# Optimization experiments

Hardware: AMD Instinct MI355X
Metric: run time of the kernel (lower is better)

## Reference

```python
import jax, jax.numpy as jnp
import numpy as np

VTH = 1.0          # firing threshold
SG_ALPHA = 4.0     # surrogate-gradient sharpness
TAU_MEM = 20.0

@jax.custom_vjp
def spike_fn(v):
    # Heaviside spike: 1 where membrane exceeds 0 (v is already v_mem - VTH)
    return (v > 0.0).astype(v.dtype)

def _spike_fwd(v):
    return spike_fn(v), v

def _spike_bwd(v, g):
    # sigmoid surrogate derivative: alpha * s * (1 - s)
    s = jax.nn.sigmoid(SG_ALPHA * v)
    return (g * SG_ALPHA * s * (1.0 - s),)

spike_fn.defvjp(_spike_fwd, _spike_bwd)

def lif_scan(h):
    # h: (batch, time, seq, hidden) -> spikes same shape, rate scalar
    beta = 1.0 - 1.0 / TAU_MEM  # membrane decay
    b, t, s, d = h.shape
    h_t = jnp.moveaxis(h, 1, 0)  # (time, batch, seq, hidden)

    def step(v, inp):
        v = beta * v + inp
        spk = spike_fn(v - VTH)
        v = v * (1.0 - spk)  # hard reset
        return v, spk

    v0 = jnp.zeros((b, s, d), dtype=h.dtype)
    _, spikes = jax.lax.scan(step, v0, h_t)
    spikes = jnp.moveaxis(spikes, 0, 1)  # (batch, time, seq, hidden)
    rate = spikes.mean()
    return spikes, rate

def setup_inputs() -> dict:
    key = jax.random.key(0)
    k1, k2, k3 = jax.random.split(key, 3)
    b, t, s, d = 16, 4, 256, 512
    hidden = 2048
    x = jax.random.normal(k1, (b, t, s, d), dtype=jnp.float32)
    # Kaiming-ish init so membrane inputs are O(1)
    w1 = jax.random.normal(k2, (hidden, d), dtype=jnp.float32) * (1.0 / np.sqrt(d))
    w2 = jax.random.normal(k3, (d, hidden), dtype=jnp.float32) * (1.0 / np.sqrt(hidden))
    return {"x": x, "w1": w1, "w2": w2}

def reference(x, w1, w2):
    # fc1: (b,t,s,d) @ (hidden,d)^T -> (b,t,s,hidden)
    h = jnp.einsum('btsd,hd->btsh', x, w1)
    spikes, rate = lif_scan(h)
    # fc2: (b,t,s,hidden) @ (d,hidden)^T -> (b,t,s,d)
    out = jnp.einsum('btsh,dh->btsd', spikes, w2)
    return out, rate
```

## Files before the change

kernel.cpp:

```cpp
#include <hip/hip_runtime.h>
#include <stdint.h>


typedef __attribute__((ext_vector_type(8))) short short8;
typedef __attribute__((ext_vector_type(4))) float f32x4;

#define AS1 __attribute__((address_space(1)))
#define AS3 __attribute__((address_space(3)))

__device__ __forceinline__ void load_lds16(const void* g, void* l) {
  __builtin_amdgcn_global_load_lds((const AS1 void*)g, (AS3 void*)l, 16, 0, 0);
}

__device__ __forceinline__ unsigned short f2bf(float f) {
  union { float f; unsigned u; } un; un.f = f;
  unsigned r = un.u + 0x7FFF + ((un.u >> 16) & 1);
  return (unsigned short)(r >> 16);
}
__device__ __forceinline__ float bf2f(unsigned short u) {
  union { unsigned u; float f; } un; un.u = ((unsigned)u) << 16; return un.f;
}

__global__ __launch_bounds__(256) void k0_split(
    const float* __restrict__ w2, unsigned short* __restrict__ hi,
    unsigned short* __restrict__ lo)
{
  int i = (blockIdx.x * 256 + threadIdx.x) * 4;
  float4 w = *(const float4*)&w2[i];
  unsigned short h4[4], l4[4];
  float ws[4] = {w.x, w.y, w.z, w.w};
#pragma unroll
  for (int c = 0; c < 4; ++c) {
    unsigned short h = f2bf(ws[c]);
    h4[c] = h;
    l4[c] = f2bf(ws[c] - bf2f(h));
  }
  *(ushort4*)&hi[i] = *(const ushort4*)h4;
  *(ushort4*)&lo[i] = *(const ushort4*)l4;
}

#define K1KT 32
#define SA_STR 256
#define SB_STR 128

__global__ __launch_bounds__(256, 2) void k1_gemm_lif(
    const float* __restrict__ x,
    const float* __restrict__ w1,
    unsigned short* __restrict__ spikes,
    unsigned* __restrict__ cnt_out)
{
  __shared__ float sA[K1KT * SA_STR];
  __shared__ float sB[K1KT * SB_STR];

  const int tid = threadIdx.x;
  const int tx  = tid & 15;
  const int ty  = tid >> 4;
  const int t   = ty & 3;
  const int ssg = ty >> 2;

  const int bx = blockIdx.x;
  const int b  = bx >> 2;
  const int s0 = (bx & 3) * 64;
  const int h0 = blockIdx.y * 128;

  const int u  = tid >> 3;
  const int kg = tid & 7;

  float acc[16][8];
#pragma unroll
  for (int i = 0; i < 16; ++i)
#pragma unroll
    for (int j = 0; j < 8; ++j) acc[i][j] = 0.0f;

  const int aBase  = t * 64 + ssg * 16;
  const int tXor   = 4 * t;
  const int bBase0 = tx * 4;
  const int bBase1 = 64 + tx * 4;

  for (int k0 = 0; k0 < 512; k0 += K1KT) {
    __syncthreads();

#pragma unroll
    for (int j = 0; j < 8; ++j) {
      int r  = u + 32 * j;
      int tr = r >> 6, ss = r & 63;
      size_t grow = ((size_t)(b * 4 + tr) << 8) + s0 + ss;
      float4 a = *(const float4*)&x[grow * 512 + k0 + kg * 4];
      int sl = r ^ (4 * (kg ^ tr));
      sA[(4 * kg + 0) * SA_STR + sl] = a.x;
      sA[(4 * kg + 1) * SA_STR + sl] = a.y;
      sA[(4 * kg + 2) * SA_STR + sl] = a.z;
      sA[(4 * kg + 3) * SA_STR + sl] = a.w;
    }
#pragma unroll
    for (int j = 0; j < 4; ++j) {
      int c = u + 32 * j;
      float4 wv = *(const float4*)&w1[(size_t)(h0 + c) * 512 + k0 + kg * 4];
      int sl = c ^ (4 * kg);
      sB[(4 * kg + 0) * SB_STR + sl] = wv.x;
      sB[(4 * kg + 1) * SB_STR + sl] = wv.y;
      sB[(4 * kg + 2) * SB_STR + sl] = wv.z;
      sB[(4 * kg + 3) * SB_STR + sl] = wv.w;
    }
    __syncthreads();

    for (int kk = 0; kk < K1KT; kk += 4) {
      const int aXor = kk ^ tXor;
      const int bXor = kk;
#pragma unroll
      for (int k2i = 0; k2i < 4; ++k2i) {
        const int k = kk + k2i;
        const float* aRow = &sA[k * SA_STR];
        const float* bRow = &sB[k * SB_STR];
        float4 a0 = *(const float4*)&aRow[(aBase + 0)  ^ aXor];
        float4 a1 = *(const float4*)&aRow[(aBase + 4)  ^ aXor];
        float4 a2 = *(const float4*)&aRow[(aBase + 8)  ^ aXor];
        float4 a3 = *(const float4*)&aRow[(aBase + 12) ^ aXor];
        float4 b0 = *(const float4*)&bRow[bBase0 ^ bXor];
        float4 b1 = *(const float4*)&bRow[bBase1 ^ bXor];
        float av[16] = {a0.x, a0.y, a0.z, a0.w, a1.x, a1.y, a1.z, a1.w,
                        a2.x, a2.y, a2.z, a2.w, a3.x, a3.y, a3.z, a3.w};
        float bv[8]  = {b0.x, b0.y, b0.z, b0.w, b1.x, b1.y, b1.z, b1.w};
#pragma unroll
        for (int i = 0; i < 16; ++i)
#pragma unroll
          for (int j = 0; j < 8; ++j)
            acc[i][j] = __builtin_fmaf(av[i], bv[j], acc[i][j]);
      }
    }
  }

  unsigned cnt = 0;
#pragma unroll
  for (int i = 0; i < 16; ++i) {
    unsigned short sp[8];
#pragma unroll
    for (int j = 0; j < 8; ++j) {
      float a = acc[i][j];
      float h[4];
#pragma unroll
      for (int tt = 0; tt < 4; ++tt)
        h[tt] = __shfl(a, tt * 16 + tx, 64);
      float vv = 0.0f;
      bool smine = false;
#pragma unroll
      for (int tt = 0; tt < 4; ++tt) {
        vv = __fadd_rn(__fmul_rn(0.95f, vv), h[tt]);
        bool s = vv > 1.0f;
        smine = (tt == t) ? s : smine;
        vv = s ? 0.0f : vv;
      }
      cnt += smine ? 1u : 0u;
      sp[j] = smine ? (unsigned short)0x3F80 : (unsigned short)0;
    }
    size_t grow = ((size_t)(b * 4 + t) << 8) + s0 + ssg * 16 + i;
    unsigned short* rowp = spikes + grow * 2048 + h0;
    *(ushort4*)&rowp[tx * 4]      = *(const ushort4*)&sp[0];
    *(ushort4*)&rowp[64 + tx * 4] = *(const ushort4*)&sp[4];
  }

#pragma unroll
  for (int off = 32; off; off >>= 1) cnt += __shfl_down(cnt, off);
  if ((tid & 63) == 0) atomicAdd(cnt_out, cnt);
}

__global__ __launch_bounds__(256, 2) void k2_gemm_mfma(
    const unsigned short* __restrict__ spikes,
    const unsigned short* __restrict__ w2h,
    const unsigned short* __restrict__ w2l,
    float* __restrict__ out)
{
  __shared__ alignas(16) short smA [128 * 64];
  __shared__ alignas(16) short smBh[128 * 64];
  __shared__ alignas(16) short smBl[128 * 64];

  const int tid  = threadIdx.x;
  const int lane = tid & 63;
  const int quad = lane >> 4;
  const int l15  = lane & 15;
  const int wv   = tid >> 6;
  const int wm   = wv & 1;
  const int wn   = wv >> 1;

  const size_t r0 = (size_t)blockIdx.x * 128;
  const int    d0 = blockIdx.y * 128;

  int srow[4], sg8[4];
#pragma unroll
  for (int j = 0; j < 4; ++j) {
    int gi  = j * 256 + tid;
    srow[j] = gi >> 3;
    sg8[j]  = ((gi & 7) ^ (srow[j] & 7)) * 8;
  }

  const unsigned short* ab  = spikes + r0 * 2048;
  const unsigned short* bhb = w2h + (size_t)d0 * 2048;
  const unsigned short* blb = w2l + (size_t)d0 * 2048;

  f32x4 acc[4][4] = {};

  for (int k0 = 0; k0 < 2048; k0 += 64) {
    __syncthreads();
#pragma unroll
    for (int j = 0; j < 4; ++j) {
      load_lds16(ab  + (size_t)srow[j] * 2048 + k0 + sg8[j],
                 &smA [(j * 256 + tid) * 8]);
      load_lds16(bhb + (size_t)srow[j] * 2048 + k0 + sg8[j],
                 &smBh[(j * 256 + tid) * 8]);
      load_lds16(blb + (size_t)srow[j] * 2048 + k0 + sg8[j],
                 &smBl[(j * 256 + tid) * 8]);
    }
    __syncthreads();

#pragma unroll
    for (int ks = 0; ks < 2; ++ks) {
      short8 af[4], bh[4], bl[4];
#pragma unroll
      for (int mi = 0; mi < 4; ++mi) {
        int m = wm * 64 + mi * 16 + l15;
        af[mi] = ((const short8*)smA)[m * 8 + ((ks * 4 + quad) ^ (m & 7))];
      }
#pragma unroll
      for (int ni = 0; ni < 4; ++ni) {
        int n = wn * 64 + ni * 16 + l15;
        int sl = n * 8 + ((ks * 4 + quad) ^ (n & 7));
        bh[ni] = ((const short8*)smBh)[sl];
        bl[ni] = ((const short8*)smBl)[sl];
      }
#pragma unroll
      for (int mi = 0; mi < 4; ++mi)
#pragma unroll
        for (int ni = 0; ni < 4; ++ni) {
          acc[mi][ni] = __builtin_amdgcn_mfma_f32_16x16x32_bf16(
              af[mi], bh[ni], acc[mi][ni], 0, 0, 0);
          acc[mi][ni] = __builtin_amdgcn_mfma_f32_16x16x32_bf16(
              af[mi], bl[ni], acc[mi][ni], 0, 0, 0);
        }
    }
  }

  float* ob = out + r0 * 512 + d0;
#pragma unroll
  for (int mi = 0; mi < 4; ++mi)
#pragma unroll
    for (int ni = 0; ni < 4; ++ni)
#pragma unroll
      for (int r = 0; r < 4; ++r) {
        int rr = wm * 64 + mi * 16 + quad * 4 + r;
        int cc = wn * 64 + ni * 16 + l15;
        ob[(size_t)rr * 512 + cc] = acc[mi][ni][r];
      }
}

#define KT 16
#define PADF 68

__global__ __launch_bounds__(256) void k2_gemm_valu(
    const unsigned short* __restrict__ spikes,
    const float* __restrict__ w2,
    float* __restrict__ out)
{
  __shared__ float sA[KT][PADF];
  __shared__ float sB[KT][PADF];

  const int tid = threadIdx.x;
  const int tx  = tid & 15;
  const int ty  = tid >> 4;
  const int lr  = tid >> 2;
  const int lg  = tid & 3;

  const size_t r0 = (size_t)blockIdx.x * 64;
  const int    d0 = blockIdx.y * 64;

  float acc[4][4];
#pragma unroll
  for (int i = 0; i < 4; ++i)
#pragma unroll
    for (int j = 0; j < 4; ++j) acc[i][j] = 0.0f;

  for (int k0 = 0; k0 < 2048; k0 += KT) {
    __syncthreads();
    ushort4 av = *(const ushort4*)&spikes[(r0 + lr) * 2048 + k0 + lg * 4];
    float4  bv = *(const float4*)&w2[(size_t)(d0 + lr) * 2048 + k0 + lg * 4];
    sA[lg * 4 + 0][lr] = bf2f(av.x); sA[lg * 4 + 1][lr] = bf2f(av.y);
    sA[lg * 4 + 2][lr] = bf2f(av.z); sA[lg * 4 + 3][lr] = bf2f(av.w);
    sB[lg * 4 + 0][lr] = bv.x; sB[lg * 4 + 1][lr] = bv.y;
    sB[lg * 4 + 2][lr] = bv.z; sB[lg * 4 + 3][lr] = bv.w;
    __syncthreads();

#pragma unroll
    for (int k = 0; k < KT; ++k) {
      float4 a4 = *(const float4*)&sA[k][ty * 4];
      float4 b4 = *(const float4*)&sB[k][tx * 4];
      float aa[4] = {a4.x, a4.y, a4.z, a4.w};
      float bb[4] = {b4.x, b4.y, b4.z, b4.w};
#pragma unroll
      for (int i = 0; i < 4; ++i)
#pragma unroll
        for (int j = 0; j < 4; ++j)
          acc[i][j] = __builtin_fmaf(aa[i], bb[j], acc[i][j]);
    }
  }

#pragma unroll
  for (int i = 0; i < 4; ++i) {
    float4 o = make_float4(acc[i][0], acc[i][1], acc[i][2], acc[i][3]);
    *(float4*)&out[(r0 + ty * 4 + i) * 512 + d0 + tx * 4] = o;
  }
}

__global__ void k3_rate(const unsigned* __restrict__ cnt, float* __restrict__ dst) {
  dst[0] = (float)((double)(*cnt) / 33554432.0);
}

extern "C" void kernel_launch(void* const* d_in, const int* in_sizes, int n_in,
                              void* d_out, int out_size, void* d_ws, size_t ws_size,
                              hipStream_t stream) {
  const float* x  = (const float*)d_in[0];
  const float* w1 = (const float*)d_in[1];
  const float* w2 = (const float*)d_in[2];
  float* out = (float*)d_out;

  unsigned* cnt = (unsigned*)d_ws;
  unsigned short* spikes = (unsigned short*)((char*)d_ws + 256);
  const size_t SPIKES_B = (size_t)16384 * 2048 * 2;
  unsigned short* w2h = (unsigned short*)((char*)d_ws + 256 + SPIKES_B);
  unsigned short* w2l = w2h + (size_t)512 * 2048;
  const size_t NEED_SPLIT = 256 + SPIKES_B + 2 * (size_t)512 * 2048 * 2;

  hipMemsetAsync(d_ws, 0, 256, stream);

  hipLaunchKernelGGL(k1_gemm_lif, dim3(64, 16), dim3(256), 0, stream,
                     x, w1, spikes, cnt);

  if (ws_size >= NEED_SPLIT) {
    hipLaunchKernelGGL(k0_split, dim3(1024), dim3(256), 0, stream, w2, w2h, w2l);
    hipLaunchKernelGGL(k2_gemm_mfma, dim3(128, 4), dim3(256), 0, stream,
                       spikes, w2h, w2l, out);
  } else {
    hipLaunchKernelGGL(k2_gemm_valu, dim3(256, 8), dim3(256), 0, stream,
                       spikes, w2, out);
  }

  hipLaunchKernelGGL(k3_rate, dim3(1), dim3(1), 0, stream, cnt, out + 8388608);
}
```

Measured before the change: 572.1 us.

## Shrink fc1 tile to 128x128, keep LIF time steps per thread, double occupancy

```diff
diff --git a/kernel.cpp b/kernel.cpp
--- a/kernel.cpp
+++ b/kernel.cpp
@@ -39,11 +39,11 @@
   *(ushort4*)&lo[i] = *(const ushort4*)l4;
 }
 
-#define K1KT 32
-#define SA_STR 256
-#define SB_STR 128
-
-__global__ __launch_bounds__(256, 2) void k1_gemm_lif(
+#define K1KT 16
+#define SA_STR 176
+#define SB_STR 176
+
+__global__ __launch_bounds__(256, 4) void k1_gemm_lif(
     const float* __restrict__ x,
     const float* __restrict__ w1,
     unsigned short* __restrict__ spikes,
@@ -55,108 +55,99 @@
   const int tid = threadIdx.x;
   const int tx  = tid & 15;
   const int ty  = tid >> 4;
-  const int t   = ty & 3;
-  const int ssg = ty >> 2;
 
   const int bx = blockIdx.x;
-  const int b  = bx >> 2;
-  const int s0 = (bx & 3) * 64;
+  const int b  = bx >> 3;
+  const int s0 = (bx & 7) * 32;
   const int h0 = blockIdx.y * 128;
 
-  const int u  = tid >> 3;
-  const int kg = tid & 7;
-
-  float acc[16][8];
-#pragma unroll
-  for (int i = 0; i < 16; ++i)
-#pragma unroll
-    for (int j = 0; j < 8; ++j) acc[i][j] = 0.0f;
-
-  const int aBase  = t * 64 + ssg * 16;
-  const int tXor   = 4 * t;
-  const int bBase0 = tx * 4;
-  const int bBase1 = 64 + tx * 4;
+  const int kg = tid & 3;
+  const int u  = tid >> 2;
+
+  float acc[8][8];
+#pragma unroll
+  for (int m = 0; m < 8; ++m)
+#pragma unroll
+    for (int j = 0; j < 8; ++j) acc[m][j] = 0.0f;
+
+  const size_t growA0 = ((size_t)(b * 4 + (u & 3)) << 8) + s0 + (u >> 2);
+  const size_t growA1 = growA0 + 16;
+  const float* xA0 = x  + growA0 * 512 + kg * 4;
+  const float* xA1 = x  + growA1 * 512 + kg * 4;
+  const float* wB0 = w1 + (size_t)(h0 + u) * 512 + kg * 4;
+  const float* wB1 = w1 + (size_t)(h0 + u + 64) * 512 + kg * 4;
+
+  float* sAw = &sA[(4 * kg) * SA_STR + u + 16 * kg];
+  float* sBw = &sB[(4 * kg) * SB_STR + u + 16 * kg];
+
+  const float* sAr = &sA[ty * 8];
+  const float* sBr = &sB[tx * 4];
 
   for (int k0 = 0; k0 < 512; k0 += K1KT) {
-    __syncthreads();
-
+    float4 a0v = *(const float4*)(xA0 + k0);
+    float4 a1v = *(const float4*)(xA1 + k0);
+    float4 b0v = *(const float4*)(wB0 + k0);
+    float4 b1v = *(const float4*)(wB1 + k0);
+
+    __syncthreads();
+    {
+      float a0s[4] = {a0v.x, a0v.y, a0v.z, a0v.w};
+      float a1s[4] = {a1v.x, a1v.y, a1v.z, a1v.w};
+      float b0s[4] = {b0v.x, b0v.y, b0v.z, b0v.w};
+      float b1s[4] = {b1v.x, b1v.y, b1v.z, b1v.w};
+#pragma unroll
+      for (int c = 0; c < 4; ++c) {
+        sAw[c * SA_STR]      = a0s[c];
+        sAw[c * SA_STR + 64] = a1s[c];
+        sBw[c * SB_STR]      = b0s[c];
+        sBw[c * SB_STR + 64] = b1s[c];
+      }
+    }
+    __syncthreads();
+
+#pragma unroll
+    for (int k = 0; k < K1KT; ++k) {
+      const int off = k * SA_STR + 16 * (k >> 2);
+      float4 va0 = *(const float4*)(sAr + off);
+      float4 va1 = *(const float4*)(sAr + off + 4);
+      float4 vb0 = *(const float4*)(sBr + off);
+      float4 vb1 = *(const float4*)(sBr + off + 64);
+      float av[8] = {va0.x, va0.y, va0.z, va0.w, va1.x, va1.y, va1.z, va1.w};
+      float bv[8] = {vb0.x, vb0.y, vb0.z, vb0.w, vb1.x, vb1.y, vb1.z, vb1.w};
+#pragma unroll
+      for (int m = 0; m < 8; ++m)
+#pragma unroll
+        for (int j = 0; j < 8; ++j)
+          acc[m][j] = __builtin_fmaf(av[m], bv[j], acc[m][j]);
+    }
+  }
+
+  unsigned cnt = 0;
+#pragma unroll
+  for (int i = 0; i < 2; ++i) {
+    unsigned short sp[4][8];
 #pragma unroll
     for (int j = 0; j < 8; ++j) {
-      int r  = u + 32 * j;
-      int tr = r >> 6, ss = r & 63;
-      size_t grow = ((size_t)(b * 4 + tr) << 8) + s0 + ss;
-      float4 a = *(const float4*)&x[grow * 512 + k0 + kg * 4];
-      int sl = r ^ (4 * (kg ^ tr));
-      sA[(4 * kg + 0) * SA_STR + sl] = a.x;
-      sA[(4 * kg + 1) * SA_STR + sl] = a.y;
-      sA[(4 * kg + 2) * SA_STR + sl] = a.z;
-      sA[(4 * kg + 3) * SA_STR + sl] = a.w;
-    }
-#pragma unroll
-    for (int j = 0; j < 4; ++j) {
-      int c = u + 32 * j;
-      float4 wv = *(const float4*)&w1[(size_t)(h0 + c) * 512 + k0 + kg * 4];
-      int sl = c ^ (4 * kg);
-      sB[(4 * kg + 0) * SB_STR + sl] = wv.x;
-      sB[(4 * kg + 1) * SB_STR + sl] = wv.y;
-      sB[(4 * kg + 2) * SB_STR + sl] = wv.z;
-      sB[(4 * kg + 3) * SB_STR + sl] = wv.w;
-    }
-    __syncthreads();
-
-    for (int kk = 0; kk < K1KT; kk += 4) {
-      const int aXor = kk ^ tXor;
-      const int bXor = kk;
-#pragma unroll
-      for (int k2i = 0; k2i < 4; ++k2i) {
-        const int k = kk + k2i;
-        const float* aRow = &sA[k * SA_STR];
-        const float* bRow = &sB[k * SB_STR];
-        float4 a0 = *(const float4*)&aRow[(aBase + 0)  ^ aXor];
-        float4 a1 = *(const float4*)&aRow[(aBase + 4)  ^ aXor];
-        float4 a2 = *(const float4*)&aRow[(aBase + 8)  ^ aXor];
-        float4 a3 = *(const float4*)&aRow[(aBase + 12) ^ aXor];
-        float4 b0 = *(const float4*)&bRow[bBase0 ^ bXor];
-        float4 b1 = *(const float4*)&bRow[bBase1 ^ bXor];
-        float av[16] = {a0.x, a0.y, a0.z, a0.w, a1.x, a1.y, a1.z, a1.w,
-                        a2.x, a2.y, a2.z, a2.w, a3.x, a3.y, a3.z, a3.w};
-        float bv[8]  = {b0.x, b0.y, b0.z, b0.w, b1.x, b1.y, b1.z, b1.w};
-#pragma unroll
-        for (int i = 0; i < 16; ++i)
-#pragma unroll
-          for (int j = 0; j < 8; ++j)
-            acc[i][j] = __builtin_fmaf(av[i], bv[j], acc[i][j]);
-      }
-    }
-  }
-
-  unsigned cnt = 0;
-#pragma unroll
-  for (int i = 0; i < 16; ++i) {
-    unsigned short sp[8];
-#pragma unroll
-    for (int j = 0; j < 8; ++j) {
-      float a = acc[i][j];
-      float h[4];
-#pragma unroll
-      for (int tt = 0; tt < 4; ++tt)
-        h[tt] = __shfl(a, tt * 16 + tx, 64);
-      float vv = 0.0f;
-      bool smine = false;
-#pragma unroll
-      for (int tt = 0; tt < 4; ++tt) {
-        vv = __fadd_rn(__fmul_rn(0.95f, vv), h[tt]);
+      float v = 0.0f;
+#pragma unroll
+      for (int t = 0; t < 4; ++t) {
+        float vv = __fadd_rn(__fmul_rn(0.95f, v), acc[i * 4 + t][j]);
         bool s = vv > 1.0f;
-        smine = (tt == t) ? s : smine;
-        vv = s ? 0.0f : vv;
-      }
-      cnt += smine ? 1u : 0u;
-      sp[j] = smine ? (unsigned short)0x3F80 : (unsigned short)0;
-    }
-    size_t grow = ((size_t)(b * 4 + t) << 8) + s0 + ssg * 16 + i;
-    unsigned short* rowp = spikes + grow * 2048 + h0;
-    *(ushort4*)&rowp[tx * 4]      = *(const ushort4*)&sp[0];
-    *(ushort4*)&rowp[64 + tx * 4] = *(const ushort4*)&sp[4];
+        sp[t][j] = s ? (unsigned short)0x3F80 : (unsigned short)0;
+        cnt += s ? 1u : 0u;
+        v = s ? 0.0f : vv;
+      }
+    }
+#pragma unroll
+    for (int t = 0; t < 4; ++t) {
+      size_t grow = ((size_t)(b * 4 + t) << 8) + s0 + ty * 2 + i;
+      unsigned short* rowp = spikes + grow * 2048 + h0;
+      ushort4 o0, o1;
+      o0.x = sp[t][0]; o0.y = sp[t][1]; o0.z = sp[t][2]; o0.w = sp[t][3];
+      o1.x = sp[t][4]; o1.y = sp[t][5]; o1.z = sp[t][6]; o1.w = sp[t][7];
+      *(ushort4*)&rowp[tx * 4]      = o0;
+      *(ushort4*)&rowp[64 + tx * 4] = o1;
+    }
   }
 
 #pragma unroll
@@ -330,7 +321,7 @@
 
   hipMemsetAsync(d_ws, 0, 256, stream);
 
-  hipLaunchKernelGGL(k1_gemm_lif, dim3(64, 16), dim3(256), 0, stream,
+  hipLaunchKernelGGL(k1_gemm_lif, dim3(128, 16), dim3(256), 0, stream,
                      x, w1, spikes, cnt);
 
   if (ws_size >= NEED_SPLIT) {
```

Result: faster. 511.1 us (-10.7%).
